# Kernel optimization log

Hardware: AMD Instinct MI355X
Metric: run time of the kernel (lower is better)

Reference implementation:

```python
import jax, jax.numpy as jnp
import numpy as np

# Static problem sizes (batch 'batch' vector is built as B equal-sized graphs).
B, N_PER, K = 4, 4096, 64          # graphs, points per graph, max_num_neighbors
RATIO, R = 0.25, 0.2               # fps ratio, radius
M = int(N_PER * RATIO)             # fps samples per graph (1024)
C_IN = 64                          # input feature channels
MLP_DIMS = [C_IN + 3, 64, 64, 128]


def setup_inputs() -> dict:
    key = jax.random.key(0)
    ks = jax.random.split(key, 8)
    x = jax.random.normal(ks[0], (B * N_PER, C_IN), dtype=jnp.float32)
    pos = jax.random.uniform(ks[1], (B * N_PER, 3), dtype=jnp.float32)
    batch = jnp.repeat(jnp.arange(B, dtype=jnp.int32), N_PER)

    def lin(k, fan_in, fan_out):
        s = 1.0 / np.sqrt(fan_in)
        return jax.random.uniform(k, (fan_in, fan_out), jnp.float32, -s, s)

    W1 = lin(ks[2], MLP_DIMS[0], MLP_DIMS[1]); b1 = jnp.zeros((MLP_DIMS[1],), jnp.float32)
    W2 = lin(ks[3], MLP_DIMS[1], MLP_DIMS[2]); b2 = jnp.zeros((MLP_DIMS[2],), jnp.float32)
    W3 = lin(ks[4], MLP_DIMS[2], MLP_DIMS[3]); b3 = jnp.zeros((MLP_DIMS[3],), jnp.float32)
    return {"x": x, "pos": pos, "batch": batch,
            "W1": W1, "b1": b1, "W2": W2, "b2": b2, "W3": W3, "b3": b3}


def _fps(pos_b):
    """Farthest point sampling on one graph. pos_b: [n,3] -> [M] int32 indices.
    Deterministic start at index 0 (PyG uses a random start)."""
    n = pos_b.shape[0]

    def step(carry, _):
        dists, last = carry
        d = jnp.sum((pos_b - pos_b[last]) ** 2, axis=-1)
        dists = jnp.minimum(dists, d)
        nxt = jnp.argmax(dists).astype(jnp.int32)
        return (dists, nxt), nxt

    init = (jnp.full((n,), jnp.inf, dtype=pos_b.dtype), jnp.int32(0))
    _, rest = jax.lax.scan(step, init, None, length=M - 1)
    return jnp.concatenate([jnp.zeros((1,), jnp.int32), rest])


def _radius(pos_b):
    """Radius neighbor search (self-query). Returns nbr [n,K] indices and valid [n,K] mask.
    Takes the K nearest in-ball neighbors (self always included, d=0)."""
    d2 = jnp.sum((pos_b[:, None, :] - pos_b[None, :, :]) ** 2, axis=-1)  # [n,n]
    neg = jnp.where(d2 <= R * R, -d2, -jnp.inf)
    vals, nbr = jax.lax.top_k(neg, K)
    return nbr, vals > -jnp.inf


def _pointconv(x_b, pos_b, nbr, valid, W1, b1, W2, b2, W3, b3):
    """PointConv: out_i = max_{j in N(i)} MLP(concat(x_j, pos_j - pos_i))."""
    rel = pos_b[nbr] - pos_b[:, None, :]                 # [n,K,3]
    feat = jnp.concatenate([x_b[nbr], rel], axis=-1)     # [n,K,C_IN+3]
    h = jax.nn.relu(feat @ W1 + b1)
    h = jax.nn.relu(h @ W2 + b2)
    h = jax.nn.relu(h @ W3 + b3)                          # [n,K,128]
    h = jnp.where(valid[..., None], h, -jnp.inf)          # mask padded neighbor slots
    return h.max(axis=1)                                  # [n,128]; self-edge guarantees validity


def reference(x, pos, batch, W1, b1, W2, b2, W3, b3):
    xb = x.reshape(B, N_PER, C_IN)
    pb = pos.reshape(B, N_PER, 3)
    nbr, valid = jax.vmap(_radius)(pb)                    # [B,n,K]
    out = jax.vmap(_pointconv, in_axes=(0, 0, 0, 0) + (None,) * 6)(
        xb, pb, nbr, valid, W1, b1, W2, b2, W3, b3)       # [B,n,128]
    idx = jax.vmap(_fps)(pb)                              # [B,M]
    x_s = jnp.take_along_axis(out, idx[..., None], axis=1).reshape(B * M, -1)
    pos_s = jnp.take_along_axis(pb, idx[..., None], axis=1).reshape(B * M, 3)
    batch_s = jnp.repeat(jnp.arange(B, dtype=batch.dtype), M)
    return x_s, pos_s, batch_s
```

## Files before the change

kernel.cpp:

```cpp
#include <hip/hip_runtime.h>

#define NPER 4096
#define MS   1024
#define CIN  64
#define LCAP 384

typedef float  f32x4 __attribute__((ext_vector_type(4)));
typedef short  s16x8 __attribute__((ext_vector_type(8)));

__device__ __forceinline__ float d2_exact(float ax, float ay, float az,
                                          float bx, float by, float bz) {
  float dx = __fsub_rn(ax, bx);
  float dy = __fsub_rn(ay, by);
  float dz = __fsub_rn(az, bz);
  return __fadd_rn(__fadd_rn(__fmul_rn(dx, dx), __fmul_rn(dy, dy)), __fmul_rn(dz, dz));
}

__device__ __forceinline__ unsigned short f2bf(float f) {
  unsigned b = __float_as_uint(f);
  return (unsigned short)((b + 0x7FFFu + ((b >> 16) & 1u)) >> 16);
}

template <int CTRL, int RMASK>
__device__ __forceinline__ unsigned long long dpp_max_step(unsigned long long k) {
  int hi = (int)(unsigned)(k >> 32);
  int lo = (int)(unsigned)(k & 0xFFFFFFFFull);
  int thi = __builtin_amdgcn_update_dpp(hi, hi, CTRL, RMASK, 0xF, false);
  int tlo = __builtin_amdgcn_update_dpp(lo, lo, CTRL, RMASK, 0xF, false);
  unsigned long long t =
      ((unsigned long long)(unsigned)thi << 32) | (unsigned)tlo;
  return t > k ? t : k;
}

__device__ __forceinline__ unsigned long long u64max(unsigned long long a,
                                                    unsigned long long b) {
  return a > b ? a : b;
}

__global__ __launch_bounds__(512) void fps_kernel(const float* __restrict__ pos,
                                                  int* __restrict__ idx_out) {
  const int b = blockIdx.x;
  const int t = threadIdx.x;
  __shared__ float4 s_pos4[NPER];
  __shared__ __align__(16) unsigned long long s_red[2][8];
  const float* pb = pos + (size_t)b * NPER * 3;
  for (int i = t; i < NPER; i += 512)
    s_pos4[i] = make_float4(pb[i * 3], pb[i * 3 + 1], pb[i * 3 + 2], 0.f);
  if (t == 0) idx_out[b * MS] = 0;
  __syncthreads();

  float px[8], py[8], pz[8], dist[8];
#pragma unroll
  for (int j = 0; j < 8; ++j) {
    float4 p = s_pos4[t + j * 512];
    px[j] = p.x; py[j] = p.y; pz[j] = p.z;
    dist[j] = __builtin_inff();
  }
  const int w = t >> 6;
  const int lane = t & 63;

  float lx = s_pos4[0].x, ly = s_pos4[0].y, lz = s_pos4[0].z;

  for (int m = 1; m < MS; ++m) {
    float bd = -1.0f;
    int bi = 0;
#pragma unroll
    for (int j = 0; j < 8; ++j) {
      float d2 = d2_exact(px[j], py[j], pz[j], lx, ly, lz);
      float nd = fminf(dist[j], d2);
      dist[j] = nd;
      if (nd > bd) { bd = nd; bi = t + j * 512; }
    }
    unsigned long long k =
        ((unsigned long long)__float_as_uint(bd) << 32) | (unsigned)(~bi);
    k = dpp_max_step<0x111, 0xF>(k);
    k = dpp_max_step<0x112, 0xF>(k);
    k = dpp_max_step<0x114, 0xF>(k);
    k = dpp_max_step<0x118, 0xF>(k);
    k = dpp_max_step<0x142, 0xA>(k);
    k = dpp_max_step<0x143, 0xC>(k);
    const int par = m & 1;
    if (lane == 63) s_red[par][w] = k;
    __syncthreads();
    ulonglong2 p0 = *reinterpret_cast<const ulonglong2*>(&s_red[par][0]);
    ulonglong2 p1 = *reinterpret_cast<const ulonglong2*>(&s_red[par][2]);
    ulonglong2 p2 = *reinterpret_cast<const ulonglong2*>(&s_red[par][4]);
    ulonglong2 p3 = *reinterpret_cast<const ulonglong2*>(&s_red[par][6]);
    unsigned long long a = u64max(p0.x, p0.y);
    unsigned long long c = u64max(p1.x, p1.y);
    unsigned long long d = u64max(p2.x, p2.y);
    unsigned long long e = u64max(p3.x, p3.y);
    unsigned long long kb = u64max(u64max(a, c), u64max(d, e));
    const int nx = (int)(~(unsigned)(kb & 0xFFFFFFFFull));
    if (t == 0) idx_out[b * MS + m] = nx;
    float4 wp = s_pos4[nx];
    lx = wp.x; ly = wp.y; lz = wp.z;
  }
}

__global__ __launch_bounds__(512, 4) void radconv_kernel(
    const float* __restrict__ x, const float* __restrict__ pos,
    const int* __restrict__ idx,
    const float* __restrict__ W1, const float* __restrict__ B1,
    const float* __restrict__ W2, const float* __restrict__ B2,
    const float* __restrict__ W3, const float* __restrict__ B3,
    float* __restrict__ out) {
  const int t = threadIdx.x;
  const int g = blockIdx.x >> 9;
  const int qpair = blockIdx.x & 511;
  const float* pb = pos + (size_t)g * NPER * 3;
  const float* xb = x + (size_t)g * NPER * CIN;

  __shared__ int s_cnt[2];
  __shared__ float s_ctr[2][4];
  __shared__ __align__(16) unsigned long long s_list[2][LCAP];
  __shared__ int s_nbr[2][64];
  __shared__ __align__(16) unsigned short sFeat[2][64 * 104];
  __shared__ __align__(16) unsigned short sW1[64 * 104];
  __shared__ __align__(16) unsigned short sW2[64 * 72];
  __shared__ __align__(16) unsigned short sW3[128 * 72];

  if (t < 2) s_cnt[t] = 0;
  const int q0 = g * MS + qpair * 2;
  const int qiA = idx[q0], qiB = idx[q0 + 1];
  const float cAx = pb[qiA * 3], cAy = pb[qiA * 3 + 1], cAz = pb[qiA * 3 + 2];
  const float cBx = pb[qiB * 3], cBy = pb[qiB * 3 + 1], cBz = pb[qiB * 3 + 2];
  if (t == 0) { s_ctr[0][0] = cAx; s_ctr[0][1] = cAy; s_ctr[0][2] = cAz; }
  if (t == 1) { s_ctr[1][0] = cBx; s_ctr[1][1] = cBy; s_ctr[1][2] = cBz; }
  __syncthreads();

  {
    float pp[24];
    const float4* pv = (const float4*)(pb + (size_t)t * 24);
#pragma unroll
    for (int r = 0; r < 6; ++r) {
      float4 v = pv[r];
      pp[r * 4 + 0] = v.x; pp[r * 4 + 1] = v.y;
      pp[r * 4 + 2] = v.z; pp[r * 4 + 3] = v.w;
    }
#pragma unroll
    for (int jj = 0; jj < 8; ++jj) {
      const int j = t * 8 + jj;
      const float X = pp[jj * 3], Y = pp[jj * 3 + 1], Z = pp[jj * 3 + 2];
      float dA = d2_exact(X, Y, Z, cAx, cAy, cAz);
      if (dA <= 0.04f) {
        int p = atomicAdd(&s_cnt[0], 1);
        if (p < LCAP)
          s_list[0][p] = ((unsigned long long)__float_as_uint(dA) << 32) | (unsigned)j;
      }
      float dB = d2_exact(X, Y, Z, cBx, cBy, cBz);
      if (dB <= 0.04f) {
        int p = atomicAdd(&s_cnt[1], 1);
        if (p < LCAP)
          s_list[1][p] = ((unsigned long long)__float_as_uint(dB) << 32) | (unsigned)j;
      }
    }
  }
  for (int ee = t; ee < 64 * 64; ee += 512) {
    int c = ee >> 6, kk = 67 + (ee & 63);
    if (kk < 104) sW1[c * 104 + kk] = 0;
  }
  for (int e = t; e < 67 * 64; e += 512) {
    int k = e >> 6, c = e & 63;
    sW1[c * 104 + k] = f2bf(W1[e]);
  }
  for (int e = t; e < 64 * 64; e += 512) {
    int k = e >> 6, c = e & 63;
    sW2[c * 72 + k] = f2bf(W2[e]);
  }
  for (int e = t; e < 64 * 128; e += 512) {
    int k = e >> 7, c = e & 127;
    sW3[c * 72 + k] = f2bf(W3[e]);
  }
  __syncthreads();

  const int w = t >> 6, lane = t & 63;
  const int c0 = min(min(s_cnt[0], LCAP), 64);
  const int c1 = min(min(s_cnt[1], LCAP), 64);

  {
    const int rq = w >> 2;
    const int nsurv = min(s_cnt[rq], LCAP);
    for (int e = (w & 3) * 64 + lane; e < nsurv; e += 256) {
      unsigned long long mykey = s_list[rq][e];
      int rank = 0;
      int o = 0;
      for (; o + 8 <= nsurv; o += 8) {
        unsigned long long k0 = s_list[rq][o + 0], k1 = s_list[rq][o + 1];
        unsigned long long k2 = s_list[rq][o + 2], k3 = s_list[rq][o + 3];
        unsigned long long k4 = s_list[rq][o + 4], k5 = s_list[rq][o + 5];
        unsigned long long k6 = s_list[rq][o + 6], k7 = s_list[rq][o + 7];
        rank += (k0 < mykey) + (k1 < mykey) + (k2 < mykey) + (k3 < mykey) +
                (k4 < mykey) + (k5 < mykey) + (k6 < mykey) + (k7 < mykey);
      }
      for (; o < nsurv; ++o) rank += (s_list[rq][o] < mykey) ? 1 : 0;
      if (rank < 64) s_nbr[rq][rank] = (int)(mykey & 0xFFFFFFFFull);
    }
  }
  __syncthreads();

  {
    const int slot = t >> 2, part = t & 3;
    const int gq = slot >> 6, s = slot & 63;
    const int cq = gq ? c1 : c0;
    unsigned short* frow = &sFeat[gq][s * 104];
    uint4 z; z.x = z.y = z.z = z.w = 0u;
    if (s < cq) {
      const int j = s_nbr[gq][s];
      const float4* xr = (const float4*)(xb + (size_t)j * CIN + part * 16);
      float4 v0 = xr[0], v1 = xr[1], v2 = xr[2], v3 = xr[3];
      uint4 w0, w1;
      w0.x = f2bf(v0.x) | ((unsigned)f2bf(v0.y) << 16);
      w0.y = f2bf(v0.z) | ((unsigned)f2bf(v0.w) << 16);
      w0.z = f2bf(v1.x) | ((unsigned)f2bf(v1.y) << 16);
      w0.w = f2bf(v1.z) | ((unsigned)f2bf(v1.w) << 16);
      w1.x = f2bf(v2.x) | ((unsigned)f2bf(v2.y) << 16);
      w1.y = f2bf(v2.z) | ((unsigned)f2bf(v2.w) << 16);
      w1.z = f2bf(v3.x) | ((unsigned)f2bf(v3.y) << 16);
      w1.w = f2bf(v3.z) | ((unsigned)f2bf(v3.w) << 16);
      *(uint4*)(frow + part * 16) = w0;
      *(uint4*)(frow + part * 16 + 8) = w1;
      uint4 rz = z;
      if (part == 0) {
        const float cx = gq ? cBx : cAx, cy = gq ? cBy : cAy, cz = gq ? cBz : cAz;
        rz.x = f2bf(pb[j * 3] - cx) | ((unsigned)f2bf(pb[j * 3 + 1] - cy) << 16);
        rz.y = (unsigned)f2bf(pb[j * 3 + 2] - cz);
      }
      *(uint4*)(frow + 64 + part * 8) = rz;
    } else {
      *(uint4*)(frow + part * 16) = z;
      *(uint4*)(frow + part * 16 + 8) = z;
      *(uint4*)(frow + 64 + part * 8) = z;
    }
  }
  __syncthreads();

  const int qq2 = w >> 2;
  const int mt = w & 3;
  const int lo = lane & 15, hi = lane >> 4;
  unsigned short* F = &sFeat[qq2][0];
  const int arow = (16 * mt + lo) * 104;
  const int hrow = (16 * mt + hi * 4) * 104;

  {
    f32x4 acc[4];
#pragma unroll
    for (int n = 0; n < 4; ++n) {
      float bb = B1[n * 16 + lo];
      acc[n] = (f32x4){bb, bb, bb, bb};
    }
    s16x8 a0 = *(const s16x8*)(F + arow + 0 + hi * 8);
    s16x8 a1 = *(const s16x8*)(F + arow + 32 + hi * 8);
    s16x8 a2 = *(const s16x8*)(F + arow + 64 + hi * 8);
#pragma unroll
    for (int n = 0; n < 4; ++n) {
      const unsigned short* Bp = &sW1[(n * 16 + lo) * 104 + hi * 8];
      s16x8 b0 = *(const s16x8*)(Bp);
      s16x8 b1 = *(const s16x8*)(Bp + 32);
      s16x8 b2 = *(const s16x8*)(Bp + 64);
      acc[n] = __builtin_amdgcn_mfma_f32_16x16x32_bf16(a0, b0, acc[n], 0, 0, 0);
      acc[n] = __builtin_amdgcn_mfma_f32_16x16x32_bf16(a1, b1, acc[n], 0, 0, 0);
      acc[n] = __builtin_amdgcn_mfma_f32_16x16x32_bf16(a2, b2, acc[n], 0, 0, 0);
    }
#pragma unroll
    for (int n = 0; n < 4; ++n)
#pragma unroll
      for (int r = 0; r < 4; ++r)
        F[hrow + r * 104 + n * 16 + lo] = f2bf(fmaxf(acc[n][r], 0.f));
  }
  {
    f32x4 acc[4];
#pragma unroll
    for (int n = 0; n < 4; ++n) {
      float bb = B2[n * 16 + lo];
      acc[n] = (f32x4){bb, bb, bb, bb};
    }
    s16x8 a0 = *(const s16x8*)(F + arow + 0 + hi * 8);
    s16x8 a1 = *(const s16x8*)(F + arow + 32 + hi * 8);
#pragma unroll
    for (int n = 0; n < 4; ++n) {
      const unsigned short* Bp = &sW2[(n * 16 + lo) * 72 + hi * 8];
      s16x8 b0 = *(const s16x8*)(Bp);
      s16x8 b1 = *(const s16x8*)(Bp + 32);
      acc[n] = __builtin_amdgcn_mfma_f32_16x16x32_bf16(a0, b0, acc[n], 0, 0, 0);
      acc[n] = __builtin_amdgcn_mfma_f32_16x16x32_bf16(a1, b1, acc[n], 0, 0, 0);
    }
#pragma unroll
    for (int n = 0; n < 4; ++n)
#pragma unroll
      for (int r = 0; r < 4; ++r)
        F[hrow + r * 104 + n * 16 + lo] = f2bf(fmaxf(acc[n][r], 0.f));
  }
  float pm[8];
  {
    const int cq = qq2 ? c1 : c0;
    f32x4 acc[8];
#pragma unroll
    for (int n = 0; n < 8; ++n) {
      float bb = B3[n * 16 + lo];
      acc[n] = (f32x4){bb, bb, bb, bb};
    }
    s16x8 a0 = *(const s16x8*)(F + arow + 0 + hi * 8);
    s16x8 a1 = *(const s16x8*)(F + arow + 32 + hi * 8);
#pragma unroll
    for (int n = 0; n < 8; ++n) {
      const unsigned short* Bp = &sW3[(n * 16 + lo) * 72 + hi * 8];
      s16x8 b0 = *(const s16x8*)(Bp);
      s16x8 b1 = *(const s16x8*)(Bp + 32);
      acc[n] = __builtin_amdgcn_mfma_f32_16x16x32_bf16(a0, b0, acc[n], 0, 0, 0);
      acc[n] = __builtin_amdgcn_mfma_f32_16x16x32_bf16(a1, b1, acc[n], 0, 0, 0);
    }
#pragma unroll
    for (int n = 0; n < 8; ++n) {
      float v = -1e30f;
#pragma unroll
      for (int r = 0; r < 4; ++r) {
        int row = 16 * mt + hi * 4 + r;
        if (row < cq) v = fmaxf(v, fmaxf(acc[n][r], 0.f));
      }
      pm[n] = v;
    }
  }
  __syncthreads();

  float* red = (float*)&sFeat[0][0];
#pragma unroll
  for (int n = 0; n < 8; ++n)
    red[((qq2 * 128) + n * 16 + lo) * 17 + mt * 4 + hi] = pm[n];
  __syncthreads();

  if (t < 256) {
    const int gq = t >> 7, cc = t & 127;
    const float* rp = red + (gq * 128 + cc) * 17;
    float v = rp[0];
#pragma unroll
    for (int p = 1; p < 16; ++p) v = fmaxf(v, rp[p]);
    const int qrow = q0 + gq;
    out[(size_t)qrow * 128 + cc] = v;
  }
  if (t == 256 || t == 257) {
    const int gq = t - 256;
    const int qrow = q0 + gq;
    out[524288 + qrow * 3 + 0] = s_ctr[gq][0];
    out[524288 + qrow * 3 + 1] = s_ctr[gq][1];
    out[524288 + qrow * 3 + 2] = s_ctr[gq][2];
    out[536576 + qrow] = (float)g;
  }
}

extern "C" void kernel_launch(void* const* d_in, const int* in_sizes, int n_in,
                              void* d_out, int out_size, void* d_ws, size_t ws_size,
                              hipStream_t stream) {
  const float* x   = (const float*)d_in[0];
  const float* pos = (const float*)d_in[1];
  const float* W1  = (const float*)d_in[3];
  const float* B1  = (const float*)d_in[4];
  const float* W2  = (const float*)d_in[5];
  const float* B2  = (const float*)d_in[6];
  const float* W3  = (const float*)d_in[7];
  const float* B3  = (const float*)d_in[8];
  float* out = (float*)d_out;
  int* idx = (int*)d_ws;

  fps_kernel<<<4, 512, 0, stream>>>(pos, idx);
  radconv_kernel<<<2048, 512, 0, stream>>>(x, pos, idx, W1, B1, W2, B2, W3, B3, out);
}
```

Measured before the change: 697.7 us.

## Morton-sort FPS points per thread and skip distance updates via bounding-box bound

The FPS kernel now buckets points into an 8x8x8 Morton grid with a shared histogram and scan, so each of 256 threads owns 16 spatially contiguous points. Each thread keeps a bounding box and a cached max, and skips the 16-point distance update whenever the box lower bound is no smaller than its current max distance. The packed tag carries the original index for tie-breaking and the sorted slot for lookup. The goal is to cut per-iteration ALU work and the cross-wave reduction width in the serial 1023-step loop, at the cost of setup sorting and a conservative-bound correctness risk.

```diff
diff --git a/kernel.cpp b/kernel.cpp
--- a/kernel.cpp
+++ b/kernel.cpp
@@ -37,42 +37,105 @@
   return a > b ? a : b;
 }
 
-__global__ __launch_bounds__(512) void fps_kernel(const float* __restrict__ pos,
+__global__ __launch_bounds__(256) void fps_kernel(const float* __restrict__ pos,
                                                   int* __restrict__ idx_out) {
   const int b = blockIdx.x;
   const int t = threadIdx.x;
-  __shared__ float4 s_pos4[NPER];
-  __shared__ __align__(16) unsigned long long s_red[2][8];
+  __shared__ float4 s_pts[NPER];
+  __shared__ unsigned s_hist[512];
+  __shared__ unsigned s_scan[256];
+  __shared__ float4 s_first;
+  __shared__ __align__(16) unsigned long long s_red[2][4];
   const float* pb = pos + (size_t)b * NPER * 3;
-  for (int i = t; i < NPER; i += 512)
-    s_pos4[i] = make_float4(pb[i * 3], pb[i * 3 + 1], pb[i * 3 + 2], 0.f);
+
+  float tx[16], ty[16], tz[16];
+  int mo[16];
+  s_hist[t] = 0u;
+  s_hist[t + 256] = 0u;
+  __syncthreads();
+#pragma unroll
+  for (int j = 0; j < 16; ++j) {
+    const int i = t + j * 256;
+    float X = pb[i * 3], Y = pb[i * 3 + 1], Z = pb[i * 3 + 2];
+    tx[j] = X; ty[j] = Y; tz[j] = Z;
+    int cx = min(7, max(0, (int)(X * 8.f)));
+    int cy = min(7, max(0, (int)(Y * 8.f)));
+    int cz = min(7, max(0, (int)(Z * 8.f)));
+    int m = ((cx & 1) << 2) | ((cx & 2) << 4) | ((cx & 4) << 6)
+          | ((cy & 1) << 1) | ((cy & 2) << 3) | ((cy & 4) << 5)
+          | ((cz & 1)     ) | ((cz & 2) << 2) | ((cz & 4) << 4);
+    mo[j] = m;
+    atomicAdd(&s_hist[m], 1u);
+    if (i == 0) s_first = make_float4(X, Y, Z, 0.f);
+  }
+  __syncthreads();
+  const unsigned h0 = s_hist[2 * t], h1 = s_hist[2 * t + 1];
+  const unsigned psum = h0 + h1;
+  s_scan[t] = psum;
+  __syncthreads();
+  for (int d = 1; d < 256; d <<= 1) {
+    unsigned v = (t >= d) ? s_scan[t - d] : 0u;
+    __syncthreads();
+    s_scan[t] += v;
+    __syncthreads();
+  }
+  {
+    unsigned excl = s_scan[t] - psum;
+    s_hist[2 * t] = excl;
+    s_hist[2 * t + 1] = excl + h0;
+  }
+  __syncthreads();
+#pragma unroll
+  for (int j = 0; j < 16; ++j) {
+    const int i = t + j * 256;
+    unsigned p = atomicAdd(&s_hist[mo[j]], 1u);
+    unsigned tag = ((unsigned)((~i) & 0xFFF) << 12) | p;
+    s_pts[p] = make_float4(tx[j], ty[j], tz[j], __uint_as_float(tag));
+  }
   if (t == 0) idx_out[b * MS] = 0;
   __syncthreads();
 
-  float px[8], py[8], pz[8], dist[8];
-#pragma unroll
-  for (int j = 0; j < 8; ++j) {
-    float4 p = s_pos4[t + j * 512];
-    px[j] = p.x; py[j] = p.y; pz[j] = p.z;
+  float px[16], py[16], pz[16], dist[16];
+  unsigned lw[16];
+#pragma unroll
+  for (int j = 0; j < 16; ++j) {
+    float4 p4 = s_pts[t * 16 + j];
+    px[j] = p4.x; py[j] = p4.y; pz[j] = p4.z;
+    lw[j] = __float_as_uint(p4.w);
     dist[j] = __builtin_inff();
   }
-  const int w = t >> 6;
-  const int lane = t & 63;
-
-  float lx = s_pos4[0].x, ly = s_pos4[0].y, lz = s_pos4[0].z;
+  float lox = px[0], hix = px[0], loy = py[0], hiy = py[0], loz = pz[0], hiz = pz[0];
+#pragma unroll
+  for (int j = 1; j < 16; ++j) {
+    lox = fminf(lox, px[j]); hix = fmaxf(hix, px[j]);
+    loy = fminf(loy, py[j]); hiy = fmaxf(hiy, py[j]);
+    loz = fminf(loz, pz[j]); hiz = fmaxf(hiz, pz[j]);
+  }
+  unsigned long long cache = ((unsigned long long)0x7F800000u << 32);
+
+  const int w = t >> 6, lane = t & 63;
+  float sx = s_first.x, sy = s_first.y, sz = s_first.z;
 
   for (int m = 1; m < MS; ++m) {
-    float bd = -1.0f;
-    int bi = 0;
-#pragma unroll
-    for (int j = 0; j < 8; ++j) {
-      float d2 = d2_exact(px[j], py[j], pz[j], lx, ly, lz);
-      float nd = fminf(dist[j], d2);
-      dist[j] = nd;
-      if (nd > bd) { bd = nd; bi = t + j * 512; }
-    }
-    unsigned long long k =
-        ((unsigned long long)__float_as_uint(bd) << 32) | (unsigned)(~bi);
+    const float bd = __uint_as_float((unsigned)(cache >> 32));
+    float ddx = fmaxf(fmaxf(lox - sx, sx - hix), 0.f);
+    float ddy = fmaxf(fmaxf(loy - sy, sy - hiy), 0.f);
+    float ddz = fmaxf(fmaxf(loz - sz, sz - hiz), 0.f);
+    float lb2 = (ddx * ddx + ddy * ddy) + ddz * ddz;
+    if (lb2 * 0.9999988f < bd) {
+      unsigned long long nc = 0ull;
+#pragma unroll
+      for (int j = 0; j < 16; ++j) {
+        float d2 = d2_exact(px[j], py[j], pz[j], sx, sy, sz);
+        float nd = fminf(dist[j], d2);
+        dist[j] = nd;
+        unsigned long long ck =
+            ((unsigned long long)__float_as_uint(nd) << 32) | lw[j];
+        if (ck > nc) nc = ck;
+      }
+      cache = nc;
+    }
+    unsigned long long k = cache;
     k = dpp_max_step<0x111, 0xF>(k);
     k = dpp_max_step<0x112, 0xF>(k);
     k = dpp_max_step<0x114, 0xF>(k);
@@ -82,19 +145,13 @@
     const int par = m & 1;
     if (lane == 63) s_red[par][w] = k;
     __syncthreads();
-    ulonglong2 p0 = *reinterpret_cast<const ulonglong2*>(&s_red[par][0]);
-    ulonglong2 p1 = *reinterpret_cast<const ulonglong2*>(&s_red[par][2]);
-    ulonglong2 p2 = *reinterpret_cast<const ulonglong2*>(&s_red[par][4]);
-    ulonglong2 p3 = *reinterpret_cast<const ulonglong2*>(&s_red[par][6]);
-    unsigned long long a = u64max(p0.x, p0.y);
-    unsigned long long c = u64max(p1.x, p1.y);
-    unsigned long long d = u64max(p2.x, p2.y);
-    unsigned long long e = u64max(p3.x, p3.y);
-    unsigned long long kb = u64max(u64max(a, c), u64max(d, e));
-    const int nx = (int)(~(unsigned)(kb & 0xFFFFFFFFull));
-    if (t == 0) idx_out[b * MS + m] = nx;
-    float4 wp = s_pos4[nx];
-    lx = wp.x; ly = wp.y; lz = wp.z;
+    ulonglong2 ab = *reinterpret_cast<const ulonglong2*>(&s_red[par][0]);
+    ulonglong2 cd = *reinterpret_cast<const ulonglong2*>(&s_red[par][2]);
+    unsigned long long kb = u64max(u64max(ab.x, ab.y), u64max(cd.x, cd.y));
+    const unsigned kl = (unsigned)kb;
+    if (t == 0) idx_out[b * MS + m] = 4095 - ((kl >> 12) & 0xFFF);
+    float4 wp = s_pts[kl & 0xFFF];
+    sx = wp.x; sy = wp.y; sz = wp.z;
   }
 }
 
@@ -362,6 +419,6 @@
   float* out = (float*)d_out;
   int* idx = (int*)d_ws;
 
-  fps_kernel<<<4, 512, 0, stream>>>(pos, idx);
+  fps_kernel<<<4, 256, 0, stream>>>(pos, idx);
   radconv_kernel<<<2048, 512, 0, stream>>>(x, pos, idx, W1, B1, W2, B2, W3, B3, out);
 }
```

Result: slower. 796.6 us (+14.2%).

## Fuse FPS and radius-conv into one persistent launch with progress flags

Applied to the files above, without the earlier changes.

Merges the FPS kernel and the radius/pointconv kernel into a single launch. The first four blocks to claim an atomic role counter run FPS at raised priority and publish progress every 32 samples. The remaining blocks spin until their query samples are published, then do the neighbor search and MLP. This overlaps the serial FPS with the conv work instead of running them back to back. FPS also switches to 256 threads using packed f32 add/mul, and the conv blocks now use one carved shared buffer. The cost is a memset, spin-waiting blocks that occupy compute units, and a dependence on the role blocks being scheduled first to avoid deadlock.

```diff
diff --git a/kernel.cpp b/kernel.cpp
--- a/kernel.cpp
+++ b/kernel.cpp
@@ -4,9 +4,22 @@
 #define MS   1024
 #define CIN  64
 #define LCAP 384
+#define SMB  74288
 
 typedef float  f32x4 __attribute__((ext_vector_type(4)));
+typedef float  f32x2 __attribute__((ext_vector_type(2)));
 typedef short  s16x8 __attribute__((ext_vector_type(8)));
+
+__device__ __forceinline__ f32x2 pk_add(f32x2 a, f32x2 b) {
+  f32x2 d;
+  asm("v_pk_add_f32 %0, %1, %2" : "=v"(d) : "v"(a), "v"(b));
+  return d;
+}
+__device__ __forceinline__ f32x2 pk_mul(f32x2 a, f32x2 b) {
+  f32x2 d;
+  asm("v_pk_mul_f32 %0, %1, %2" : "=v"(d) : "v"(a), "v"(b));
+  return d;
+}
 
 __device__ __forceinline__ float d2_exact(float ax, float ay, float az,
                                           float bx, float by, float bz) {
@@ -37,122 +50,152 @@
   return a > b ? a : b;
 }
 
-__global__ __launch_bounds__(512) void fps_kernel(const float* __restrict__ pos,
-                                                  int* __restrict__ idx_out) {
-  const int b = blockIdx.x;
-  const int t = threadIdx.x;
-  __shared__ float4 s_pos4[NPER];
-  __shared__ __align__(16) unsigned long long s_red[2][8];
-  const float* pb = pos + (size_t)b * NPER * 3;
-  for (int i = t; i < NPER; i += 512)
-    s_pos4[i] = make_float4(pb[i * 3], pb[i * 3 + 1], pb[i * 3 + 2], 0.f);
-  if (t == 0) idx_out[b * MS] = 0;
-  __syncthreads();
-
-  float px[8], py[8], pz[8], dist[8];
-#pragma unroll
-  for (int j = 0; j < 8; ++j) {
-    float4 p = s_pos4[t + j * 512];
-    px[j] = p.x; py[j] = p.y; pz[j] = p.z;
-    dist[j] = __builtin_inff();
-  }
-  const int w = t >> 6;
-  const int lane = t & 63;
-
-  float lx = s_pos4[0].x, ly = s_pos4[0].y, lz = s_pos4[0].z;
-
-  for (int m = 1; m < MS; ++m) {
-    float bd = -1.0f;
-    int bi = 0;
-#pragma unroll
-    for (int j = 0; j < 8; ++j) {
-      float d2 = d2_exact(px[j], py[j], pz[j], lx, ly, lz);
-      float nd = fminf(dist[j], d2);
-      dist[j] = nd;
-      if (nd > bd) { bd = nd; bi = t + j * 512; }
-    }
-    unsigned long long k =
-        ((unsigned long long)__float_as_uint(bd) << 32) | (unsigned)(~bi);
-    k = dpp_max_step<0x111, 0xF>(k);
-    k = dpp_max_step<0x112, 0xF>(k);
-    k = dpp_max_step<0x114, 0xF>(k);
-    k = dpp_max_step<0x118, 0xF>(k);
-    k = dpp_max_step<0x142, 0xA>(k);
-    k = dpp_max_step<0x143, 0xC>(k);
-    const int par = m & 1;
-    if (lane == 63) s_red[par][w] = k;
-    __syncthreads();
-    ulonglong2 p0 = *reinterpret_cast<const ulonglong2*>(&s_red[par][0]);
-    ulonglong2 p1 = *reinterpret_cast<const ulonglong2*>(&s_red[par][2]);
-    ulonglong2 p2 = *reinterpret_cast<const ulonglong2*>(&s_red[par][4]);
-    ulonglong2 p3 = *reinterpret_cast<const ulonglong2*>(&s_red[par][6]);
-    unsigned long long a = u64max(p0.x, p0.y);
-    unsigned long long c = u64max(p1.x, p1.y);
-    unsigned long long d = u64max(p2.x, p2.y);
-    unsigned long long e = u64max(p3.x, p3.y);
-    unsigned long long kb = u64max(u64max(a, c), u64max(d, e));
-    const int nx = (int)(~(unsigned)(kb & 0xFFFFFFFFull));
-    if (t == 0) idx_out[b * MS + m] = nx;
-    float4 wp = s_pos4[nx];
-    lx = wp.x; ly = wp.y; lz = wp.z;
-  }
-}
-
-__global__ __launch_bounds__(512, 4) void radconv_kernel(
+__global__ __launch_bounds__(512, 4) void fused_kernel(
     const float* __restrict__ x, const float* __restrict__ pos,
-    const int* __restrict__ idx,
     const float* __restrict__ W1, const float* __restrict__ B1,
     const float* __restrict__ W2, const float* __restrict__ B2,
     const float* __restrict__ W3, const float* __restrict__ B3,
-    float* __restrict__ out) {
+    float* __restrict__ out, int* __restrict__ idxp, int* __restrict__ ctrl) {
   const int t = threadIdx.x;
-  const int g = blockIdx.x >> 9;
-  const int qpair = blockIdx.x & 511;
+  __shared__ __align__(16) char smraw[SMB];
+  __shared__ int s_role;
+
+  if (t == 0) s_role = atomicAdd(&ctrl[0], 1);
+  __syncthreads();
+  const int role = s_role;
+  const int w = t >> 6, lane = t & 63;
+
+  if (role < 4) {
+    __builtin_amdgcn_s_setprio(3);
+    const int b = role;
+    float4* s_pos4 = (float4*)smraw;
+    unsigned long long* s_red = (unsigned long long*)(smraw + 65536);
+    const float* pb = pos + (size_t)b * NPER * 3;
+    for (int i = t; i < NPER; i += 512)
+      s_pos4[i] = make_float4(pb[i * 3], pb[i * 3 + 1], pb[i * 3 + 2], 0.f);
+    if (t == 0) idxp[b * MS] = 0;
+    __syncthreads();
+
+    f32x2 npx[8], npy[8], npz[8], dist2[8];
+    if (t < 256) {
+#pragma unroll
+      for (int p = 0; p < 8; ++p) {
+        float4 a = s_pos4[t + (2 * p) * 256];
+        float4 c = s_pos4[t + (2 * p + 1) * 256];
+        npx[p] = (f32x2){-a.x, -c.x};
+        npy[p] = (f32x2){-a.y, -c.y};
+        npz[p] = (f32x2){-a.z, -c.z};
+        dist2[p] = (f32x2){__builtin_inff(), __builtin_inff()};
+      }
+    }
+    float sx = s_pos4[0].x, sy = s_pos4[0].y, sz = s_pos4[0].z;
+
+    for (int m = 1; m < MS; ++m) {
+      const int par = m & 1;
+      if (t < 256) {
+        float bd = -1.0f;
+        int bi = 0;
+        f32x2 sxx = (f32x2){sx, sx}, syy = (f32x2){sy, sy}, szz = (f32x2){sz, sz};
+#pragma unroll
+        for (int p = 0; p < 8; ++p) {
+          f32x2 dx = pk_add(sxx, npx[p]);
+          f32x2 dy = pk_add(syy, npy[p]);
+          f32x2 dz = pk_add(szz, npz[p]);
+          f32x2 d2 = pk_add(pk_add(pk_mul(dx, dx), pk_mul(dy, dy)), pk_mul(dz, dz));
+          float n0 = fminf(dist2[p][0], d2[0]);
+          float n1 = fminf(dist2[p][1], d2[1]);
+          dist2[p][0] = n0;
+          dist2[p][1] = n1;
+          if (n0 > bd) { bd = n0; bi = t + (2 * p) * 256; }
+          if (n1 > bd) { bd = n1; bi = t + (2 * p + 1) * 256; }
+        }
+        unsigned long long k =
+            ((unsigned long long)__float_as_uint(bd) << 32) | (unsigned)(~bi);
+        k = dpp_max_step<0x111, 0xF>(k);
+        k = dpp_max_step<0x112, 0xF>(k);
+        k = dpp_max_step<0x114, 0xF>(k);
+        k = dpp_max_step<0x118, 0xF>(k);
+        k = dpp_max_step<0x142, 0xA>(k);
+        k = dpp_max_step<0x143, 0xC>(k);
+        if (lane == 63) s_red[par * 4 + w] = k;
+      }
+      __syncthreads();
+      if (t < 256) {
+        ulonglong2 ab = *reinterpret_cast<const ulonglong2*>(&s_red[par * 4 + 0]);
+        ulonglong2 cd = *reinterpret_cast<const ulonglong2*>(&s_red[par * 4 + 2]);
+        unsigned long long kb = u64max(u64max(ab.x, ab.y), u64max(cd.x, cd.y));
+        const int nx = (int)(~(unsigned)(kb & 0xFFFFFFFFull));
+        if (t == 0) {
+          idxp[b * MS + m] = nx;
+          if ((m & 31) == 31) {
+            __threadfence();
+            atomicExch(&ctrl[1 + b], m + 1);
+          }
+        }
+        float4 wp = s_pos4[nx];
+        sx = wp.x; sy = wp.y; sz = wp.z;
+      }
+    }
+    return;
+  }
+
+  const int pp = role - 4;
+  const int g = pp >> 9;
+  const int qpair = pp & 511;
   const float* pb = pos + (size_t)g * NPER * 3;
   const float* xb = x + (size_t)g * NPER * CIN;
 
-  __shared__ int s_cnt[2];
-  __shared__ float s_ctr[2][4];
-  __shared__ __align__(16) unsigned long long s_list[2][LCAP];
-  __shared__ int s_nbr[2][64];
-  __shared__ __align__(16) unsigned short sFeat[2][64 * 104];
-  __shared__ __align__(16) unsigned short sW1[64 * 104];
-  __shared__ __align__(16) unsigned short sW2[64 * 72];
-  __shared__ __align__(16) unsigned short sW3[128 * 72];
-
+  unsigned short* sFeat = (unsigned short*)smraw;
+  unsigned short* sW1 = (unsigned short*)(smraw + 26624);
+  unsigned short* sW2 = (unsigned short*)(smraw + 39936);
+  unsigned short* sW3 = (unsigned short*)(smraw + 49152);
+  unsigned long long* s_list = (unsigned long long*)(smraw + 67584);
+  int* s_nbr = (int*)(smraw + 73728);
+  int* s_cnt = (int*)(smraw + 74240);
+  float* s_ctr = (float*)(smraw + 74248);
+  int* s_qi = (int*)(smraw + 74280);
+
+  const int q0 = g * MS + qpair * 2;
+  if (t == 0) {
+    const int need = qpair * 2 + 2;
+    while (atomicAdd(&ctrl[1 + g], 0) < need) __builtin_amdgcn_s_sleep(32);
+    s_qi[0] = atomicAdd(&idxp[q0], 0);
+    s_qi[1] = atomicAdd(&idxp[q0 + 1], 0);
+  }
   if (t < 2) s_cnt[t] = 0;
-  const int q0 = g * MS + qpair * 2;
-  const int qiA = idx[q0], qiB = idx[q0 + 1];
+  __syncthreads();
+
+  const int qiA = s_qi[0], qiB = s_qi[1];
   const float cAx = pb[qiA * 3], cAy = pb[qiA * 3 + 1], cAz = pb[qiA * 3 + 2];
   const float cBx = pb[qiB * 3], cBy = pb[qiB * 3 + 1], cBz = pb[qiB * 3 + 2];
-  if (t == 0) { s_ctr[0][0] = cAx; s_ctr[0][1] = cAy; s_ctr[0][2] = cAz; }
-  if (t == 1) { s_ctr[1][0] = cBx; s_ctr[1][1] = cBy; s_ctr[1][2] = cBz; }
-  __syncthreads();
-
-  {
-    float pp[24];
+  if (t == 0) { s_ctr[0] = cAx; s_ctr[1] = cAy; s_ctr[2] = cAz; }
+  if (t == 1) { s_ctr[4] = cBx; s_ctr[5] = cBy; s_ctr[6] = cBz; }
+
+  {
+    float ppt[24];
     const float4* pv = (const float4*)(pb + (size_t)t * 24);
 #pragma unroll
     for (int r = 0; r < 6; ++r) {
       float4 v = pv[r];
-      pp[r * 4 + 0] = v.x; pp[r * 4 + 1] = v.y;
-      pp[r * 4 + 2] = v.z; pp[r * 4 + 3] = v.w;
+      ppt[r * 4 + 0] = v.x; ppt[r * 4 + 1] = v.y;
+      ppt[r * 4 + 2] = v.z; ppt[r * 4 + 3] = v.w;
     }
 #pragma unroll
     for (int jj = 0; jj < 8; ++jj) {
       const int j = t * 8 + jj;
-      const float X = pp[jj * 3], Y = pp[jj * 3 + 1], Z = pp[jj * 3 + 2];
+      const float X = ppt[jj * 3], Y = ppt[jj * 3 + 1], Z = ppt[jj * 3 + 2];
       float dA = d2_exact(X, Y, Z, cAx, cAy, cAz);
       if (dA <= 0.04f) {
         int p = atomicAdd(&s_cnt[0], 1);
         if (p < LCAP)
-          s_list[0][p] = ((unsigned long long)__float_as_uint(dA) << 32) | (unsigned)j;
+          s_list[p] = ((unsigned long long)__float_as_uint(dA) << 32) | (unsigned)j;
       }
       float dB = d2_exact(X, Y, Z, cBx, cBy, cBz);
       if (dB <= 0.04f) {
         int p = atomicAdd(&s_cnt[1], 1);
         if (p < LCAP)
-          s_list[1][p] = ((unsigned long long)__float_as_uint(dB) << 32) | (unsigned)j;
+          s_list[LCAP + p] =
+              ((unsigned long long)__float_as_uint(dB) << 32) | (unsigned)j;
       }
     }
   }
@@ -174,27 +217,27 @@
   }
   __syncthreads();
 
-  const int w = t >> 6, lane = t & 63;
   const int c0 = min(min(s_cnt[0], LCAP), 64);
   const int c1 = min(min(s_cnt[1], LCAP), 64);
 
   {
     const int rq = w >> 2;
+    const unsigned long long* L = s_list + rq * LCAP;
     const int nsurv = min(s_cnt[rq], LCAP);
     for (int e = (w & 3) * 64 + lane; e < nsurv; e += 256) {
-      unsigned long long mykey = s_list[rq][e];
+      unsigned long long mykey = L[e];
       int rank = 0;
       int o = 0;
       for (; o + 8 <= nsurv; o += 8) {
-        unsigned long long k0 = s_list[rq][o + 0], k1 = s_list[rq][o + 1];
-        unsigned long long k2 = s_list[rq][o + 2], k3 = s_list[rq][o + 3];
-        unsigned long long k4 = s_list[rq][o + 4], k5 = s_list[rq][o + 5];
-        unsigned long long k6 = s_list[rq][o + 6], k7 = s_list[rq][o + 7];
+        unsigned long long k0 = L[o + 0], k1 = L[o + 1];
+        unsigned long long k2 = L[o + 2], k3 = L[o + 3];
+        unsigned long long k4 = L[o + 4], k5 = L[o + 5];
+        unsigned long long k6 = L[o + 6], k7 = L[o + 7];
         rank += (k0 < mykey) + (k1 < mykey) + (k2 < mykey) + (k3 < mykey) +
                 (k4 < mykey) + (k5 < mykey) + (k6 < mykey) + (k7 < mykey);
       }
-      for (; o < nsurv; ++o) rank += (s_list[rq][o] < mykey) ? 1 : 0;
-      if (rank < 64) s_nbr[rq][rank] = (int)(mykey & 0xFFFFFFFFull);
+      for (; o < nsurv; ++o) rank += (L[o] < mykey) ? 1 : 0;
+      if (rank < 64) s_nbr[rq * 64 + rank] = (int)(mykey & 0xFFFFFFFFull);
     }
   }
   __syncthreads();
@@ -203,10 +246,10 @@
     const int slot = t >> 2, part = t & 3;
     const int gq = slot >> 6, s = slot & 63;
     const int cq = gq ? c1 : c0;
-    unsigned short* frow = &sFeat[gq][s * 104];
+    unsigned short* frow = sFeat + gq * 6656 + s * 104;
     uint4 z; z.x = z.y = z.z = z.w = 0u;
     if (s < cq) {
-      const int j = s_nbr[gq][s];
+      const int j = s_nbr[gq * 64 + s];
       const float4* xr = (const float4*)(xb + (size_t)j * CIN + part * 16);
       float4 v0 = xr[0], v1 = xr[1], v2 = xr[2], v3 = xr[3];
       uint4 w0, w1;
@@ -238,7 +281,7 @@
   const int qq2 = w >> 2;
   const int mt = w & 3;
   const int lo = lane & 15, hi = lane >> 4;
-  unsigned short* F = &sFeat[qq2][0];
+  unsigned short* F = sFeat + qq2 * 6656;
   const int arow = (16 * mt + lo) * 104;
   const int hrow = (16 * mt + hi * 4) * 104;
 
@@ -323,7 +366,7 @@
   }
   __syncthreads();
 
-  float* red = (float*)&sFeat[0][0];
+  float* red = (float*)sFeat;
 #pragma unroll
   for (int n = 0; n < 8; ++n)
     red[((qq2 * 128) + n * 16 + lo) * 17 + mt * 4 + hi] = pm[n];
@@ -335,15 +378,14 @@
     float v = rp[0];
 #pragma unroll
     for (int p = 1; p < 16; ++p) v = fmaxf(v, rp[p]);
-    const int qrow = q0 + gq;
-    out[(size_t)qrow * 128 + cc] = v;
+    out[(size_t)(q0 + gq) * 128 + cc] = v;
   }
   if (t == 256 || t == 257) {
     const int gq = t - 256;
     const int qrow = q0 + gq;
-    out[524288 + qrow * 3 + 0] = s_ctr[gq][0];
-    out[524288 + qrow * 3 + 1] = s_ctr[gq][1];
-    out[524288 + qrow * 3 + 2] = s_ctr[gq][2];
+    out[524288 + qrow * 3 + 0] = s_ctr[gq * 4 + 0];
+    out[524288 + qrow * 3 + 1] = s_ctr[gq * 4 + 1];
+    out[524288 + qrow * 3 + 2] = s_ctr[gq * 4 + 2];
     out[536576 + qrow] = (float)g;
   }
 }
@@ -361,7 +403,9 @@
   const float* B3  = (const float*)d_in[8];
   float* out = (float*)d_out;
   int* idx = (int*)d_ws;
-
-  fps_kernel<<<4, 512, 0, stream>>>(pos, idx);
-  radconv_kernel<<<2048, 512, 0, stream>>>(x, pos, idx, W1, B1, W2, B2, W3, B3, out);
-}
+  int* ctrl = idx + 4096;
+
+  hipMemsetAsync(ctrl, 0, 20, stream);
+  fused_kernel<<<2052, 512, 0, stream>>>(x, pos, W1, B1, W2, B2, W3, B3,
+                                         out, idx, ctrl);
+}
```

New measurement: 773.1 us. +10.8%, slower.
